# Performance work log

Measured on AMD Instinct MI355X. Metric: run time of the kernel, lower is better.

The kernel has to match this reference:

```python
import jax, jax.numpy as jnp
import numpy as np

N_NODES = 100000
N_EDGES = 3200000
NFEAT = 256
NCLASS = 64


def setup_inputs() -> dict:
    key = jax.random.key(0)
    k1, k2, k3 = jax.random.split(key, 3)
    x = jax.random.normal(k1, (N_NODES, NFEAT), dtype=jnp.float32)
    W = jax.random.normal(k2, (NFEAT, NCLASS), dtype=jnp.float32) * (1.0 / np.sqrt(NFEAT))
    b = jnp.zeros((NCLASS,), dtype=jnp.float32)
    edge_index = jax.random.randint(k3, (2, N_EDGES), 0, N_NODES, dtype=jnp.int64)
    return {"x": x, "W": W, "b": b, "edge_index": edge_index}


def reference(x, W, b, edge_index):
    # GCNConv (PyG defaults): add self-loops, symmetric D^-1/2 A D^-1/2 norm,
    # linear transform, bias.
    n = x.shape[0]
    loops = jnp.arange(n, dtype=edge_index.dtype)
    src = jnp.concatenate([edge_index[0], loops])  # [E+N]
    dst = jnp.concatenate([edge_index[1], loops])
    ew = jnp.ones(src.shape[0], dtype=x.dtype)
    deg = jax.ops.segment_sum(ew, dst, num_segments=n)  # in-degree incl. self-loop
    dinv = jnp.where(deg > 0, jax.lax.rsqrt(deg), 0.0)
    norm = dinv[src] * dinv[dst]  # [E+N]
    xw = x @ W  # [N, nclass] -- transform before aggregation (small out dim)
    msg = xw[src] * norm[:, None]  # gather + scale
    out = jax.ops.segment_sum(msg, dst, num_segments=n)  # scatter-add
    return out + b
```

## Files before the change

kernel.cpp:

```cpp
#include <hip/hip_runtime.h>
#include <hip/hip_fp16.h>

#define NF 256
#define NC 64
#define BINSZ 64
#define CAP 2368
#define EPB 8192
#define KC 64
#define SCAN_CHUNK 1024


__device__ inline float2 unpack_h2(unsigned int u) {
    __half2 h;
    *reinterpret_cast<unsigned int*>(&h) = u;
    return __half22float2(h);
}
__device__ inline unsigned int pack_h2(float a, float b) {
    __half2 h = __floats2half2_rn(a, b);
    return *reinterpret_cast<unsigned int*>(&h);
}

__global__ __launch_bounds__(256) void k_zcur(int* __restrict__ cursor, int nbin) {
    int i = blockIdx.x * blockDim.x + threadIdx.x;
    if (i < nbin) cursor[i] = 0;
}

__global__ __launch_bounds__(256) void k_bin(const int* __restrict__ src,
                                             const int* __restrict__ dst,
                                             int* __restrict__ cursor,
                                             int* __restrict__ binned,
                                             int ne, int nbin) {
    extern __shared__ int lds[];
    int* lcnt  = lds;
    int* lbase = lds + nbin;
    int t = threadIdx.x;
    for (int i = t; i < nbin; i += 256) lcnt[i] = 0;
    __syncthreads();

    int base = blockIdx.x * EPB;
    int lim = ne - base; if (lim > EPB) lim = EPB;

    for (int k = t; k < lim; k += 256)
        atomicAdd(&lcnt[dst[base + k] >> 6], 1);
    __syncthreads();

    for (int i = t; i < nbin; i += 256) {
        int c = lcnt[i];
        lbase[i] = (c > 0) ? atomicAdd(&cursor[i], c) : 0;
    }
    __syncthreads();
    for (int i = t; i < nbin; i += 256) lcnt[i] = 0;
    __syncthreads();

    for (int k = t; k < lim; k += 256) {
        int d = dst[base + k];
        int s = src[base + k];
        int bin = d >> 6;
        int ofs = lbase[bin] + atomicAdd(&lcnt[bin], 1);
        if (ofs < CAP) binned[(long)bin * CAP + ofs] = (s << 6) | (d & 63);
    }
}

__global__ __launch_bounds__(256) void k_binsort(const int* __restrict__ cursor,
                                                 int* __restrict__ binned,
                                                 int* __restrict__ counts,
                                                 int* __restrict__ rowstart,
                                                 int n) {
    __shared__ int sarr[CAP];
    __shared__ int sout[CAP];
    __shared__ int hist[BINSZ];
    __shared__ int lcur[BINSZ];
    int bin = blockIdx.x;
    int t = threadIdx.x;
    if (t < BINSZ) hist[t] = 0;
    __syncthreads();

    int m = cursor[bin]; if (m > CAP) m = CAP;
    int* seg = binned + (long)bin * CAP;

    for (int k = t; k < m; k += 256) {
        int e = seg[k];
        sarr[k] = e;
        atomicAdd(&hist[e & 63], 1);
    }
    __syncthreads();

    if (t < BINSZ) {
        int v = hist[t];
        int inc = v;
#pragma unroll
        for (int off = 1; off < BINSZ; off <<= 1) {
            int u = __shfl_up(inc, off);
            if (t >= off) inc += u;
        }
        int excl = inc - v;
        lcur[t] = excl;
        int node = bin * BINSZ + t;
        if (node < n) {
            counts[node]   = v;
            rowstart[node] = bin * CAP + excl;
        }
    }
    __syncthreads();

    for (int k = t; k < m; k += 256) {
        int e = sarr[k];
        int pos = atomicAdd(&lcur[e & 63], 1);
        sout[pos] = e >> 6;
    }
    __syncthreads();

    for (int k = t; k < m; k += 256) seg[k] = sout[k];
}

__global__ __launch_bounds__(256) void k_xw2h(const float* __restrict__ x,
                                              const float* __restrict__ W,
                                              const int* __restrict__ counts,
                                              unsigned int* __restrict__ xwsh, int n) {
    __shared__ float xs[KC][64];
    int t = threadIdx.x;
    int r  = t & 63;
    int cg = __builtin_amdgcn_readfirstlane(t >> 6);
    int rowbase = blockIdx.x * 64;
    int row = rowbase + r;

    float acc[16];
#pragma unroll
    for (int i = 0; i < 16; ++i) acc[i] = 0.0f;

    const float* wp = W + cg * 16;

    int srow = t >> 2, kq = t & 3;
    const float* xg = x + (size_t)(rowbase + srow) * NF;
    bool sv = (rowbase + srow) < n;

    for (int k0 = 0; k0 < NF; k0 += KC) {
        __syncthreads();
#pragma unroll
        for (int j = 0; j < 4; ++j) {
            int kk = kq * 4 + j * 16;
            float4 v;
            if (sv) v = *reinterpret_cast<const float4*>(xg + k0 + kk);
            else    { v.x = v.y = v.z = v.w = 0.0f; }
            xs[kk + 0][srow] = v.x;
            xs[kk + 1][srow] = v.y;
            xs[kk + 2][srow] = v.z;
            xs[kk + 3][srow] = v.w;
        }
        __syncthreads();
#pragma unroll 4
        for (int k = 0; k < KC; ++k) {
            float xv = xs[k][r];
            const float* wk = wp + (size_t)(k0 + k) * NC;
#pragma unroll
            for (int c = 0; c < 16; ++c)
                acc[c] = fmaf(xv, wk[c], acc[c]);
        }
    }

    if (row < n) {
        float di = rsqrtf((float)counts[row] + 1.0f);
        unsigned int buf[8];
#pragma unroll
        for (int i = 0; i < 8; ++i)
            buf[i] = pack_h2(acc[2 * i] * di, acc[2 * i + 1] * di);
        uint4* o = reinterpret_cast<uint4*>(xwsh + (size_t)row * 32 + cg * 8);
        o[0] = make_uint4(buf[0], buf[1], buf[2], buf[3]);
        o[1] = make_uint4(buf[4], buf[5], buf[6], buf[7]);
    }
}

__global__ __launch_bounds__(256) void k_gather_h(const int* __restrict__ rowstart,
                                                  const int* __restrict__ counts,
                                                  const int* __restrict__ csr,
                                                  const unsigned int* __restrict__ xwsh,
                                                  const float* __restrict__ b,
                                                  float* __restrict__ out, int n) {
    int w = (blockIdx.x * blockDim.x + threadIdx.x) >> 6;
    int lane = threadIdx.x & 63;
    if (w >= n) return;
    int half = lane >> 5;
    int lc   = lane & 31;
    int cnt = counts[w];
    int beg = rowstart[w];
    int end = beg + cnt;

    float ax = 0.0f, ay = 0.0f;
    int j = beg;
    for (; j + 8 <= end; j += 8) {
        int s0 = csr[j + 0 + half];
        int s1 = csr[j + 2 + half];
        int s2 = csr[j + 4 + half];
        int s3 = csr[j + 6 + half];
        unsigned int u0 = xwsh[(size_t)s0 * 32 + lc];
        unsigned int u1 = xwsh[(size_t)s1 * 32 + lc];
        unsigned int u2 = xwsh[(size_t)s2 * 32 + lc];
        unsigned int u3 = xwsh[(size_t)s3 * 32 + lc];
        float2 f0 = unpack_h2(u0);
        float2 f1 = unpack_h2(u1);
        float2 f2 = unpack_h2(u2);
        float2 f3 = unpack_h2(u3);
        ax += f0.x; ay += f0.y;
        ax += f1.x; ay += f1.y;
        ax += f2.x; ay += f2.y;
        ax += f3.x; ay += f3.y;
    }
    for (; j < end; j += 2) {
        int jj = j + half;
        unsigned int u = 0;
        if (jj < end) u = xwsh[(size_t)csr[jj] * 32 + lc];
        float2 f = unpack_h2(u);
        ax += f.x; ay += f.y;
    }
    ax += __shfl_xor(ax, 32);
    ay += __shfl_xor(ay, 32);
    float2 sv = unpack_h2(xwsh[(size_t)w * 32 + lc]);
    ax += sv.x; ay += sv.y;

    float di = rsqrtf((float)cnt + 1.0f);
    if (half == 0) {
        float2 o;
        o.x = ax * di + b[2 * lc + 0];
        o.y = ay * di + b[2 * lc + 1];
        *reinterpret_cast<float2*>(out + (size_t)w * NC + 2 * lc) = o;
    }
}


__global__ __launch_bounds__(256) void k_zero(int* __restrict__ p, int n) {
    int i = blockIdx.x * blockDim.x + threadIdx.x;
    if (i < n) p[i] = 0;
}

__global__ __launch_bounds__(256) void k_count(const int* __restrict__ dst,
                                               int* __restrict__ counts, int ne) {
    int e = blockIdx.x * blockDim.x + threadIdx.x;
    if (e < ne) atomicAdd(&counts[dst[e]], 1);
}

__global__ __launch_bounds__(256) void k_scan1(const int* __restrict__ counts,
                                               int* __restrict__ excl,
                                               int* __restrict__ bsum, int n) {
    __shared__ int s[256];
    int t = threadIdx.x;
    int base = blockIdx.x * SCAN_CHUNK + t * 4;
    int v[4];
    int sum = 0;
#pragma unroll
    for (int k = 0; k < 4; ++k) {
        int idx = base + k;
        v[k] = (idx < n) ? counts[idx] : 0;
        sum += v[k];
    }
    s[t] = sum;
    __syncthreads();
#pragma unroll
    for (int off = 1; off < 256; off <<= 1) {
        int xv = (t >= off) ? s[t - off] : 0;
        __syncthreads();
        s[t] += xv;
        __syncthreads();
    }
    int excl_t = s[t] - sum;
    if (t == 255) bsum[blockIdx.x] = s[t];
    int run = excl_t;
#pragma unroll
    for (int k = 0; k < 4; ++k) {
        int idx = base + k;
        if (idx < n) { excl[idx] = run; run += v[k]; }
    }
}

__global__ void k_scan2(int* __restrict__ bsum, int nblk) {
    if (threadIdx.x == 0 && blockIdx.x == 0) {
        int run = 0;
        for (int i = 0; i < nblk; ++i) { int t = bsum[i]; bsum[i] = run; run += t; }
    }
}

__global__ __launch_bounds__(256) void k_scan3(int* __restrict__ rowptr,
                                               const int* __restrict__ bsum, int n) {
    int i = blockIdx.x * blockDim.x + threadIdx.x;
    if (i < n) rowptr[i] += bsum[i / SCAN_CHUNK];
}

__global__ __launch_bounds__(256) void k_fill(const int* __restrict__ src,
                                              const int* __restrict__ dst,
                                              int* __restrict__ rowptr,
                                              int* __restrict__ csr, int ne) {
    int e = blockIdx.x * blockDim.x + threadIdx.x;
    if (e < ne) {
        int pos = atomicAdd(&rowptr[dst[e]], 1);
        csr[pos] = src[e];
    }
}

__global__ __launch_bounds__(256) void k_xw(const float* __restrict__ x,
                                            const float* __restrict__ W,
                                            const int* __restrict__ counts,
                                            float* __restrict__ xws, int n) {
    int r = blockIdx.x * blockDim.x + threadIdx.x;
    if (r >= n) return;
    float acc[NC];
#pragma unroll
    for (int c = 0; c < NC; ++c) acc[c] = 0.0f;
    const float4* xr = reinterpret_cast<const float4*>(x + (size_t)r * NF);
#pragma unroll 1
    for (int k4 = 0; k4 < NF / 4; ++k4) {
        float4 xv = xr[k4];
        const float* wk = W + (size_t)(k4 * 4) * NC;
#pragma unroll
        for (int c = 0; c < NC; ++c) {
            float a = acc[c];
            a = fmaf(xv.x, wk[0 * NC + c], a);
            a = fmaf(xv.y, wk[1 * NC + c], a);
            a = fmaf(xv.z, wk[2 * NC + c], a);
            a = fmaf(xv.w, wk[3 * NC + c], a);
            acc[c] = a;
        }
    }
    float di = rsqrtf((float)counts[r] + 1.0f);
    float4* xo = reinterpret_cast<float4*>(xws + (size_t)r * NC);
#pragma unroll
    for (int c4 = 0; c4 < NC / 4; ++c4) {
        float4 v;
        v.x = acc[4 * c4 + 0] * di;
        v.y = acc[4 * c4 + 1] * di;
        v.z = acc[4 * c4 + 2] * di;
        v.w = acc[4 * c4 + 3] * di;
        xo[c4] = v;
    }
}

__global__ __launch_bounds__(256) void k_gather(const int* __restrict__ rowend,
                                                const int* __restrict__ counts,
                                                const int* __restrict__ csr,
                                                const float* __restrict__ xws,
                                                const float* __restrict__ b,
                                                float* __restrict__ out, int n) {
    int w = (blockIdx.x * blockDim.x + threadIdx.x) >> 6;
    int lane = threadIdx.x & 63;
    if (w >= n) return;
    int cnt = counts[w];
    int end = rowend[w];
    int beg = end - cnt;

    float acc = xws[(size_t)w * NC + lane];
    int j = beg;
    for (; j + 4 <= end; j += 4) {
        int s0 = csr[j + 0], s1 = csr[j + 1], s2 = csr[j + 2], s3 = csr[j + 3];
        float v0 = xws[(size_t)s0 * NC + lane];
        float v1 = xws[(size_t)s1 * NC + lane];
        float v2 = xws[(size_t)s2 * NC + lane];
        float v3 = xws[(size_t)s3 * NC + lane];
        acc += v0; acc += v1; acc += v2; acc += v3;
    }
    for (; j < end; ++j) acc += xws[(size_t)csr[j] * NC + lane];

    float di = rsqrtf((float)cnt + 1.0f);
    out[(size_t)w * NC + lane] = acc * di + b[lane];
}

extern "C" void kernel_launch(void* const* d_in, const int* in_sizes, int n_in,
                              void* d_out, int out_size, void* d_ws, size_t ws_size,
                              hipStream_t stream) {
    const float* x = (const float*)d_in[0];
    const float* W = (const float*)d_in[1];
    const float* b = (const float*)d_in[2];
    const int*   ei = (const int*)d_in[3];
    float* out = (float*)d_out;

    int n  = in_sizes[0] / NF;
    int ne = in_sizes[3] / 2;
    const int* src = ei;
    const int* dst = ei + ne;

    int nbin = (n + BINSZ - 1) / BINSZ;

    size_t curB  = ((size_t)nbin * 4 + 4095) & ~(size_t)4095;
    size_t binB  = (size_t)nbin * CAP * 4;
    size_t cntB  = ((size_t)n * 4 + 4095) & ~(size_t)4095;
    size_t needP = curB + binB + 2 * cntB + (size_t)n * NC * 2;

    if (ws_size >= needP) {
        char* wsb = (char*)d_ws;
        int*   cursor   = (int*)(wsb);
        int*   binned   = (int*)(wsb + curB);
        int*   counts   = (int*)(wsb + curB + binB);
        int*   rowstart = (int*)(wsb + curB + binB + cntB);
        unsigned int* xwsh = (unsigned int*)(wsb + curB + binB + 2 * cntB);

        size_t ldsBin = (size_t)2 * nbin * 4;
        k_zcur    <<<(nbin + 255) / 256, 256, 0, stream>>>(cursor, nbin);
        k_bin     <<<(ne + EPB - 1) / EPB, 256, ldsBin, stream>>>(src, dst, cursor, binned, ne, nbin);
        k_binsort <<<nbin, 256, 0, stream>>>(cursor, binned, counts, rowstart, n);
        k_xw2h    <<<(n + 63) / 64, 256, 0, stream>>>(x, W, counts, xwsh, n);
        k_gather_h<<<((size_t)n * 64 + 255) / 256, 256, 0, stream>>>(rowstart, counts, binned, xwsh, b, out, n);
        return;
    }

    size_t cntB2  = (size_t)n * 4;
    size_t bsumB  = 4096;
    size_t csrOff = 2 * cntB2 + bsumB;
    size_t xwsOff = csrOff + (size_t)ne * 4;
    char* wsb = (char*)d_ws;
    int*   counts = (int*)(wsb);
    int*   rowptr = (int*)(wsb + cntB2);
    int*   bsum   = (int*)(wsb + 2 * cntB2);
    int*   csr    = (int*)(wsb + csrOff);
    float* xws    = (float*)(wsb + xwsOff);
    int nblk = (n + SCAN_CHUNK - 1) / SCAN_CHUNK;

    k_zero  <<<(n + 255) / 256, 256, 0, stream>>>(counts, n);
    k_count <<<(ne + 255) / 256, 256, 0, stream>>>(dst, counts, ne);
    k_scan1 <<<nblk, 256, 0, stream>>>(counts, rowptr, bsum, n);
    k_scan2 <<<1, 64, 0, stream>>>(bsum, nblk);
    k_scan3 <<<(n + 255) / 256, 256, 0, stream>>>(rowptr, bsum, n);
    k_xw    <<<(n + 255) / 256, 256, 0, stream>>>(x, W, counts, xws, n);
    k_fill  <<<(ne + 255) / 256, 256, 0, stream>>>(src, dst, rowptr, csr, ne);
    k_gather<<<((size_t)n * 64 + 255) / 256, 256, 0, stream>>>(rowptr, counts, csr, xws, b, out, n);
}
```

Measured before the change: 193.2 us.

## Stage edges in LDS during binning to read edge arrays once

```diff
diff --git a/kernel.cpp b/kernel.cpp
--- a/kernel.cpp
+++ b/kernel.cpp
@@ -5,7 +5,7 @@
 #define NC 64
 #define BINSZ 64
 #define CAP 2368
-#define EPB 8192
+#define EPB2 2048
 #define KC 64
 #define SCAN_CHUNK 1024
 
@@ -25,39 +25,45 @@
     if (i < nbin) cursor[i] = 0;
 }
 
-__global__ __launch_bounds__(256) void k_bin(const int* __restrict__ src,
-                                             const int* __restrict__ dst,
-                                             int* __restrict__ cursor,
-                                             int* __restrict__ binned,
-                                             int ne, int nbin) {
+__global__ __launch_bounds__(256) void k_bin2(const int* __restrict__ src,
+                                              const int* __restrict__ dst,
+                                              int* __restrict__ cursor,
+                                              int* __restrict__ binned,
+                                              int ne, int nbin) {
     extern __shared__ int lds[];
-    int* lcnt  = lds;
-    int* lbase = lds + nbin;
+    int* lcnt = lds;
+    int* spk  = lds + nbin;
+    unsigned short* sbin  = (unsigned short*)(spk + EPB2);
+    unsigned short* slofs = sbin + EPB2;
+
     int t = threadIdx.x;
     for (int i = t; i < nbin; i += 256) lcnt[i] = 0;
     __syncthreads();
 
-    int base = blockIdx.x * EPB;
-    int lim = ne - base; if (lim > EPB) lim = EPB;
-
-    for (int k = t; k < lim; k += 256)
-        atomicAdd(&lcnt[dst[base + k] >> 6], 1);
-    __syncthreads();
-
-    for (int i = t; i < nbin; i += 256) {
-        int c = lcnt[i];
-        lbase[i] = (c > 0) ? atomicAdd(&cursor[i], c) : 0;
-    }
-    __syncthreads();
-    for (int i = t; i < nbin; i += 256) lcnt[i] = 0;
-    __syncthreads();
+    int base = blockIdx.x * EPB2;
+    int lim = ne - base; if (lim > EPB2) lim = EPB2;
 
     for (int k = t; k < lim; k += 256) {
         int d = dst[base + k];
         int s = src[base + k];
         int bin = d >> 6;
-        int ofs = lbase[bin] + atomicAdd(&lcnt[bin], 1);
-        if (ofs < CAP) binned[(long)bin * CAP + ofs] = (s << 6) | (d & 63);
+        int lofs = atomicAdd(&lcnt[bin], 1);
+        spk[k]   = (s << 6) | (d & 63);
+        sbin[k]  = (unsigned short)bin;
+        slofs[k] = (unsigned short)lofs;
+    }
+    __syncthreads();
+
+    for (int i = t; i < nbin; i += 256) {
+        int c = lcnt[i];
+        lcnt[i] = (c > 0) ? atomicAdd(&cursor[i], c) : 0;
+    }
+    __syncthreads();
+
+    for (int k = t; k < lim; k += 256) {
+        int bin = sbin[k];
+        int pos = lcnt[bin] + slofs[k];
+        if (pos < CAP) binned[(long)bin * CAP + pos] = spk[k];
     }
 }
 
@@ -390,9 +396,9 @@
         int*   rowstart = (int*)(wsb + curB + binB + cntB);
         unsigned int* xwsh = (unsigned int*)(wsb + curB + binB + 2 * cntB);
 
-        size_t ldsBin = (size_t)2 * nbin * 4;
+        size_t ldsBin = (size_t)nbin * 4 + (size_t)EPB2 * 8;
         k_zcur    <<<(nbin + 255) / 256, 256, 0, stream>>>(cursor, nbin);
-        k_bin     <<<(ne + EPB - 1) / EPB, 256, ldsBin, stream>>>(src, dst, cursor, binned, ne, nbin);
+        k_bin2    <<<(ne + EPB2 - 1) / EPB2, 256, ldsBin, stream>>>(src, dst, cursor, binned, ne, nbin);
         k_binsort <<<nbin, 256, 0, stream>>>(cursor, binned, counts, rowstart, n);
         k_xw2h    <<<(n + 63) / 64, 256, 0, stream>>>(x, W, counts, xwsh, n);
         k_gather_h<<<((size_t)n * 64 + 255) / 256, 256, 0, stream>>>(rowstart, counts, binned, xwsh, b, out, n);
```

Result: slower. 224.6 us (+16.3%).

## Widen destination bins to 256 nodes and stage edges in LDS during binning

Applied to the files above, without the earlier changes.

```diff
diff --git a/kernel.cpp b/kernel.cpp
--- a/kernel.cpp
+++ b/kernel.cpp
@@ -3,8 +3,8 @@
 
 #define NF 256
 #define NC 64
-#define BINSZ 64
-#define CAP 2368
+#define BINSZ 256
+#define CAP 8832
 #define EPB 8192
 #define KC 64
 #define SCAN_CHUNK 1024
@@ -25,39 +25,43 @@
     if (i < nbin) cursor[i] = 0;
 }
 
-__global__ __launch_bounds__(256) void k_bin(const int* __restrict__ src,
-                                             const int* __restrict__ dst,
-                                             int* __restrict__ cursor,
-                                             int* __restrict__ binned,
-                                             int ne, int nbin) {
+__global__ __launch_bounds__(256) void k_bin3(const int* __restrict__ src,
+                                              const int* __restrict__ dst,
+                                              int* __restrict__ cursor,
+                                              int* __restrict__ binned,
+                                              int ne, int nbin) {
     extern __shared__ int lds[];
-    int* lcnt  = lds;
-    int* lbase = lds + nbin;
+    int* lcnt = lds;
+    int* spk  = lds + nbin;
+    unsigned short* sbin = (unsigned short*)(spk + EPB);
+
     int t = threadIdx.x;
     for (int i = t; i < nbin; i += 256) lcnt[i] = 0;
     __syncthreads();
 
     int base = blockIdx.x * EPB;
     int lim = ne - base; if (lim > EPB) lim = EPB;
-
-    for (int k = t; k < lim; k += 256)
-        atomicAdd(&lcnt[dst[base + k] >> 6], 1);
-    __syncthreads();
-
-    for (int i = t; i < nbin; i += 256) {
-        int c = lcnt[i];
-        lbase[i] = (c > 0) ? atomicAdd(&cursor[i], c) : 0;
-    }
-    __syncthreads();
-    for (int i = t; i < nbin; i += 256) lcnt[i] = 0;
-    __syncthreads();
 
     for (int k = t; k < lim; k += 256) {
         int d = dst[base + k];
         int s = src[base + k];
-        int bin = d >> 6;
-        int ofs = lbase[bin] + atomicAdd(&lcnt[bin], 1);
-        if (ofs < CAP) binned[(long)bin * CAP + ofs] = (s << 6) | (d & 63);
+        int bin = d >> 8;
+        atomicAdd(&lcnt[bin], 1);
+        spk[k]  = (s << 8) | (d & 255);
+        sbin[k] = (unsigned short)bin;
+    }
+    __syncthreads();
+
+    for (int i = t; i < nbin; i += 256) {
+        int c = lcnt[i];
+        lcnt[i] = (c > 0) ? atomicAdd(&cursor[i], c) : 0;
+    }
+    __syncthreads();
+
+    for (int k = t; k < lim; k += 256) {
+        int bin = sbin[k];
+        int pos = atomicAdd(&lcnt[bin], 1);
+        if (pos < CAP) binned[(long)bin * CAP + pos] = spk[k];
     }
 }
 
@@ -67,12 +71,12 @@
                                                  int* __restrict__ rowstart,
                                                  int n) {
     __shared__ int sarr[CAP];
-    __shared__ int sout[CAP];
     __shared__ int hist[BINSZ];
     __shared__ int lcur[BINSZ];
+    __shared__ int stmp[256];
     int bin = blockIdx.x;
     int t = threadIdx.x;
-    if (t < BINSZ) hist[t] = 0;
+    hist[t] = 0;
     __syncthreads();
 
     int m = cursor[bin]; if (m > CAP) m = CAP;
@@ -81,36 +85,34 @@
     for (int k = t; k < m; k += 256) {
         int e = seg[k];
         sarr[k] = e;
-        atomicAdd(&hist[e & 63], 1);
-    }
-    __syncthreads();
-
-    if (t < BINSZ) {
-        int v = hist[t];
-        int inc = v;
-#pragma unroll
-        for (int off = 1; off < BINSZ; off <<= 1) {
-            int u = __shfl_up(inc, off);
-            if (t >= off) inc += u;
-        }
-        int excl = inc - v;
-        lcur[t] = excl;
-        int node = bin * BINSZ + t;
-        if (node < n) {
-            counts[node]   = v;
-            rowstart[node] = bin * CAP + excl;
-        }
+        atomicAdd(&hist[e & 255], 1);
+    }
+    __syncthreads();
+
+    int v = hist[t];
+    stmp[t] = v;
+    __syncthreads();
+#pragma unroll
+    for (int off = 1; off < 256; off <<= 1) {
+        int u = (t >= off) ? stmp[t - off] : 0;
+        __syncthreads();
+        stmp[t] += u;
+        __syncthreads();
+    }
+    int excl = stmp[t] - v;
+    lcur[t] = excl;
+    int node = bin * BINSZ + t;
+    if (node < n) {
+        counts[node]   = v;
+        rowstart[node] = bin * CAP + excl;
     }
     __syncthreads();
 
     for (int k = t; k < m; k += 256) {
         int e = sarr[k];
-        int pos = atomicAdd(&lcur[e & 63], 1);
-        sout[pos] = e >> 6;
-    }
-    __syncthreads();
-
-    for (int k = t; k < m; k += 256) seg[k] = sout[k];
+        int pos = atomicAdd(&lcur[e & 255], 1);
+        seg[pos] = e >> 8;
+    }
 }
 
 __global__ __launch_bounds__(256) void k_xw2h(const float* __restrict__ x,
@@ -390,9 +392,9 @@
         int*   rowstart = (int*)(wsb + curB + binB + cntB);
         unsigned int* xwsh = (unsigned int*)(wsb + curB + binB + 2 * cntB);
 
-        size_t ldsBin = (size_t)2 * nbin * 4;
+        size_t ldsBin = (size_t)nbin * 4 + (size_t)EPB * 4 + (size_t)EPB * 2;
         k_zcur    <<<(nbin + 255) / 256, 256, 0, stream>>>(cursor, nbin);
-        k_bin     <<<(ne + EPB - 1) / EPB, 256, ldsBin, stream>>>(src, dst, cursor, binned, ne, nbin);
+        k_bin3    <<<(ne + EPB - 1) / EPB, 256, ldsBin, stream>>>(src, dst, cursor, binned, ne, nbin);
         k_binsort <<<nbin, 256, 0, stream>>>(cursor, binned, counts, rowstart, n);
         k_xw2h    <<<(n + 63) / 64, 256, 0, stream>>>(x, W, counts, xwsh, n);
         k_gather_h<<<((size_t)n * 64 + 255) / 256, 256, 0, stream>>>(rowstart, counts, binned, xwsh, b, out, n);
```

Result: no change. 189.6 us (-1.9%).
